# Performance work log

Hardware: AMD Instinct MI355X
Metric: run time of the kernel (lower is better)

## Reference

```python
import jax, jax.numpy as jnp
import numpy as np

B, S, HID = 2, 2048, 2048
NH, NKV, HD = 8, 2, 256
EPS = 1e-6
ROPE_THETA = 1e6


def _rms_norm(x, w):
    # Gemma3nRMSNorm: computed in fp32, x / sqrt(mean(x^2) + eps) * w
    xf = x.astype(jnp.float32)
    out = xf * jax.lax.rsqrt(jnp.mean(xf * xf, axis=-1, keepdims=True) + EPS) * w
    return out.astype(x.dtype)


def _rotate_half(x):
    x1, x2 = jnp.split(x, 2, axis=-1)
    return jnp.concatenate((-x2, x1), axis=-1)


def _apply_rope(x, cos, sin):
    # x: [B, S, H, D]; cos/sin: [B, S, D] -> unsqueeze head dim (unsqueeze_dim=2)
    c = cos[:, :, None, :]
    s = sin[:, :, None, :]
    return x * c + _rotate_half(x) * s


def setup_inputs() -> dict:
    key = jax.random.key(0)
    ks = jax.random.split(key, 6)
    hidden_states = jax.random.normal(ks[0], (B, S, HID), dtype=jnp.float32)
    # RoPE tables (theta = 1e6, Gemma3n)
    inv_freq = 1.0 / (ROPE_THETA ** (np.arange(0, HD, 2, dtype=np.float32) / HD))
    pos = np.arange(S, dtype=np.float32)
    freqs = pos[:, None] * inv_freq[None, :]            # [S, D/2]
    emb = np.concatenate([freqs, freqs], axis=-1)        # [S, D]
    cos = jnp.broadcast_to(jnp.asarray(np.cos(emb)), (B, S, HD)).astype(jnp.float32)
    sin = jnp.broadcast_to(jnp.asarray(np.sin(emb)), (B, S, HD)).astype(jnp.float32)
    # additive causal mask [B, 1, S, S]
    causal = jnp.tril(jnp.ones((S, S), dtype=bool))
    attention_mask = jnp.where(causal, 0.0, -1e9).astype(jnp.float32)
    attention_mask = jnp.broadcast_to(attention_mask[None, None], (B, 1, S, S))
    std = 0.02
    Wq = jax.random.normal(ks[1], (NH * HD, HID), dtype=jnp.float32) * std
    Wk = jax.random.normal(ks[2], (NKV * HD, HID), dtype=jnp.float32) * std
    Wv = jax.random.normal(ks[3], (NKV * HD, HID), dtype=jnp.float32) * std
    Wo = jax.random.normal(ks[4], (HID, NH * HD), dtype=jnp.float32) * std
    q_norm_w = jnp.ones((HD,), dtype=jnp.float32)
    k_norm_w = jnp.ones((HD,), dtype=jnp.float32)
    return {
        "hidden_states": hidden_states, "cos": cos, "sin": sin,
        "attention_mask": attention_mask,
        "Wq": Wq, "Wk": Wk, "Wv": Wv, "Wo": Wo,
        "q_norm_w": q_norm_w, "k_norm_w": k_norm_w,
    }


def reference(hidden_states, cos, sin, attention_mask, Wq, Wk, Wv, Wo, q_norm_w, k_norm_w):
    b, s, _ = hidden_states.shape
    # projections (no bias)
    q = (hidden_states @ Wq.T).reshape(b, s, NH, HD)
    k = (hidden_states @ Wk.T).reshape(b, s, NKV, HD)
    v = (hidden_states @ Wv.T).reshape(b, s, NKV, HD)
    # QK-norm then RoPE; v_norm has no scale (weight = 1)
    q = _apply_rope(_rms_norm(q, q_norm_w), cos, sin)
    k = _apply_rope(_rms_norm(k, k_norm_w), cos, sin)
    v = _rms_norm(v, jnp.float32(1.0))
    q = q.transpose(0, 2, 1, 3)  # [B, NH, S, D]
    k = k.transpose(0, 2, 1, 3)  # [B, NKV, S, D]
    v = v.transpose(0, 2, 1, 3)
    # repeat_kv: NKV -> NH (n_rep = NH // NKV)
    n_rep = NH // NKV
    k = jnp.repeat(k, n_rep, axis=1)
    v = jnp.repeat(v, n_rep, axis=1)
    # eager attention, scaling = 1.0 (as in Gemma3nTextAttention), no softcap
    scores = jnp.einsum("bhqd,bhkd->bhqk", q, k) + attention_mask
    probs = jax.nn.softmax(scores.astype(jnp.float32), axis=-1).astype(q.dtype)
    out = jnp.einsum("bhqk,bhkd->bqhd", probs, v).reshape(b, s, NH * HD)
    return out @ Wo.T
```

## Files before the change

kernel.cpp:

```cpp
#include <hip/hip_runtime.h>
#include <hip/hip_bf16.h>
#include <stdint.h>

#define S_LEN 2048
#define HIDN  2048
#define NH    8
#define NKV   2
#define HD    256

typedef _Float16 v8h  __attribute__((ext_vector_type(8)));
typedef float    v4f  __attribute__((ext_vector_type(4)));
typedef float    v16f __attribute__((ext_vector_type(16)));
typedef unsigned short u16;

struct alignas(8) US4 { u16 x, y, z, w; };

__device__ __forceinline__ u16 f2h(float f) {
  union { _Float16 h; u16 u; } t; t.h = (_Float16)f; return t.u;
}
__device__ __forceinline__ float h2f(u16 u) {
  union { _Float16 h; u16 u; } t; t.u = u; return (float)t.h;
}
__device__ __forceinline__ uint32_t pk2(float a, float b) {
  return (uint32_t)f2h(a) | ((uint32_t)f2h(b) << 16);
}

template <typename T>
__device__ __forceinline__ void gload16(const T* g, void* l) {
  __builtin_amdgcn_global_load_lds(
      (const __attribute__((address_space(1))) void*)g,
      (__attribute__((address_space(3))) void*)l, 16, 0, 0);
}

__device__ __forceinline__ void cvt_quad(const float* src, u16* dst) {
  float4 v = *reinterpret_cast<const float4*>(src);
  US4 o; o.x = f2h(v.x); o.y = f2h(v.y); o.z = f2h(v.z); o.w = f2h(v.w);
  *reinterpret_cast<US4*>(dst) = o;
}

__global__ void cvt_all_kernel(
    const float* __restrict__ hs, const float* __restrict__ Wq,
    const float* __restrict__ Wk, const float* __restrict__ Wv,
    const float* __restrict__ Wo,
    u16* __restrict__ hs_f, u16* __restrict__ w_f, u16* __restrict__ wo_f) {
  int j = blockIdx.x * blockDim.x + threadIdx.x;
  if (j < 2097152) { cvt_quad(hs + (size_t)j * 4, hs_f + (size_t)j * 4); return; }
  j -= 2097152;
  if (j < 1048576) { cvt_quad(Wq + (size_t)j * 4, w_f + (size_t)j * 4); return; }
  j -= 1048576;
  if (j < 262144) { cvt_quad(Wk + (size_t)j * 4, w_f + 4194304 + (size_t)j * 4); return; }
  j -= 262144;
  if (j < 262144) { cvt_quad(Wv + (size_t)j * 4, w_f + 5242880 + (size_t)j * 4); return; }
  j -= 262144;
  cvt_quad(Wo + (size_t)j * 4, wo_f + (size_t)j * 4);
}

template <int MF, int NFR, int OUT_F16>
__global__ __launch_bounds__(512, 2) void gemm256(
    const u16* __restrict__ A, const u16* __restrict__ Bm,
    void* __restrict__ C, int M, int N, int K) {
  __shared__ u16 As[2][MF * 2048];
  __shared__ u16 Bs[2][NFR * 4096];
  const int tid = threadIdx.x;
  const int w = tid >> 6, lane = tid & 63;
  const int wm = w >> 2, wn = w & 3;
  const int lr = lane & 15, ls = lane >> 4;
  const int m0 = blockIdx.x * (MF * 32);
  const int n0 = blockIdx.y * (NFR * 64);
  const int KT = K >> 6;
  constexpr int FPP = MF / 4;
  v4f acc[MF][NFR] = {};

  auto stageA = [&](int kt, int buf, int r) {
    const int idx = r * 512 + tid;
    const int row = idx >> 3, sp = idx & 7;
    const int sl = sp ^ (row & 7);
    gload16(A + (size_t)(m0 + row) * K + kt * 64 + sl * 8, (char*)As[buf] + idx * 16);
  };
  auto stageB = [&](int kt, int buf, int r) {
    const int idx = r * 512 + tid;
    const int row = idx >> 3, sp = idx & 7;
    const int sl = sp ^ (row & 7);
    gload16(Bm + (size_t)(n0 + row) * K + kt * 64 + sl * 8, (char*)Bs[buf] + idx * 16);
  };

#pragma unroll
  for (int r = 0; r < MF / 2; r++) stageA(0, 0, r);
#pragma unroll
  for (int r = 0; r < NFR; r++) stageB(0, 0, r);
  asm volatile("s_waitcnt vmcnt(0)" ::: "memory");
  __builtin_amdgcn_s_barrier();
  __builtin_amdgcn_sched_barrier(0);

  for (int kt = 0; kt < KT; kt++) {
    const int buf = kt & 1;
    v8h bfrag[2][NFR];
#pragma unroll
    for (int p = 0; p < 4; p++) {
      if (p == 0) {
#pragma unroll
        for (int kk = 0; kk < 2; kk++)
#pragma unroll
          for (int j = 0; j < NFR; j++) {
            const int row = wn * (NFR * 16) + j * 16 + lr;
            const int sp = (kk * 4 + ls) ^ (row & 7);
            bfrag[kk][j] = *reinterpret_cast<const v8h*>(&Bs[buf][row * 64 + sp * 8]);
          }
      }
      v8h a2[FPP][2];
#pragma unroll
      for (int ii = 0; ii < FPP; ii++)
#pragma unroll
        for (int kk = 0; kk < 2; kk++) {
          const int row = wm * MF * 16 + (p * FPP + ii) * 16 + lr;
          const int sp = (kk * 4 + ls) ^ (row & 7);
          a2[ii][kk] = *reinterpret_cast<const v8h*>(&As[buf][row * 64 + sp * 8]);
        }
      if (kt + 1 < KT) {
        if (p == 0) {
#pragma unroll
          for (int r = 0; r < MF / 2; r++) stageA(kt + 1, buf ^ 1, r);
        }
        if (p == 1) {
#pragma unroll
          for (int r = 0; r < NFR; r++) stageB(kt + 1, buf ^ 1, r);
        }
      }
      if (p == 3) asm volatile("s_waitcnt vmcnt(0)" ::: "memory");
      __builtin_amdgcn_s_barrier();
      asm volatile("s_waitcnt lgkmcnt(0)" ::: "memory");
      __builtin_amdgcn_sched_barrier(0);
      __builtin_amdgcn_s_setprio(1);
#pragma unroll
      for (int ii = 0; ii < FPP; ii++)
#pragma unroll
        for (int j = 0; j < NFR; j++)
#pragma unroll
          for (int kk = 0; kk < 2; kk++)
            acc[p * FPP + ii][j] = __builtin_amdgcn_mfma_f32_16x16x32_f16(
                a2[ii][kk], bfrag[kk][j], acc[p * FPP + ii][j], 0, 0, 0);
      __builtin_amdgcn_s_setprio(0);
      __builtin_amdgcn_s_barrier();
    }
  }

#pragma unroll
  for (int i = 0; i < MF; i++)
#pragma unroll
    for (int j = 0; j < NFR; j++) {
      const int col = n0 + wn * (NFR * 16) + j * 16 + lr;
#pragma unroll
      for (int jj = 0; jj < 4; jj++) {
        const int row = m0 + wm * MF * 16 + i * 16 + ls * 4 + jj;
        if (OUT_F16) ((u16*)C)[(size_t)row * N + col] = f2h(acc[i][j][jj]);
        else         ((float*)C)[(size_t)row * N + col] = acc[i][j][jj];
      }
    }
}

__global__ __launch_bounds__(256, 4) void norm_rope_kernel(
    const u16* __restrict__ qkv, const float* __restrict__ cosb, const float* __restrict__ sinb,
    const float* __restrict__ qw, const float* __restrict__ kw,
    u16* __restrict__ q_t, u16* __restrict__ k_t, u16* __restrict__ v_t) {
  const int task = blockIdx.x * 4 + (threadIdx.x >> 6);
  const int lane = threadIdx.x & 63;
  const int unit = task % 12;
  const int ms = task / 12;
  const int b = ms >> 11, s = ms & 2047;
  const int d0 = lane << 2;
  const int col0 = (unit < 8) ? unit * 256 : 2048 + (unit - 8) * 256;
  const US4 xv = *reinterpret_cast<const US4*>(qkv + (size_t)ms * 3072 + col0 + d0);
  float x[4] = { h2f(xv.x), h2f(xv.y), h2f(xv.z), h2f(xv.w) };
  float ss = x[0]*x[0] + x[1]*x[1] + x[2]*x[2] + x[3]*x[3];
#pragma unroll
  for (int m = 1; m < 64; m <<= 1) ss += __shfl_xor(ss, m, 64);
  const float r = rsqrtf(ss * (1.0f / 256.0f) + 1e-6f);
  if (unit < 10) {
    const float4 wv = *reinterpret_cast<const float4*>(((unit < 8) ? qw : kw) + d0);
    float xn[4];
    xn[0] = x[0] * r * wv.x; xn[1] = x[1] * r * wv.y;
    xn[2] = x[2] * r * wv.z; xn[3] = x[3] * r * wv.w;
    float rot[4];
#pragma unroll
    for (int j = 0; j < 4; j++) {
      const float p = __shfl(xn[j], lane ^ 32, 64);
      rot[j] = (lane < 32) ? -p : p;
    }
    const float4 c  = *reinterpret_cast<const float4*>(cosb + (size_t)ms * 256 + d0);
    const float4 sn = *reinterpret_cast<const float4*>(sinb + (size_t)ms * 256 + d0);
    US4 o;
    o.x = f2h(xn[0] * c.x + rot[0] * sn.x);
    o.y = f2h(xn[1] * c.y + rot[1] * sn.y);
    o.z = f2h(xn[2] * c.z + rot[2] * sn.z);
    o.w = f2h(xn[3] * c.w + rot[3] * sn.w);
    if (unit < 8) {
      const size_t dst = ((size_t)(b * NH + unit) * S_LEN + s) * 256 + d0;
      *reinterpret_cast<US4*>(q_t + dst) = o;
    } else {
      const size_t dst = ((size_t)(b * NKV + (unit - 8)) * S_LEN + s) * 256 + d0;
      *reinterpret_cast<US4*>(k_t + dst) = o;
    }
  } else {
    const int kvh = unit - 10;
    u16* vt = v_t + (size_t)(b * NKV + kvh) * 256 * 2048;
#pragma unroll
    for (int j = 0; j < 4; j++)
      vt[(size_t)(d0 + j) * 2048 + s] = f2h(x[j] * r);
  }
}

__device__ __forceinline__ void stage_kv(
    const u16* __restrict__ kb, const u16* __restrict__ vb, int kt,
    u16* Kbuf, u16* Vbuf, int tid) {
#pragma unroll
  for (int it = 0; it < 4; it++) {
    const int i1 = tid + it * 512;
    const int kv = i1 >> 5, sp = i1 & 31;
    const int sl = sp ^ (kv & 31);
    gload16(kb + (size_t)(kt * 64 + kv) * 256 + sl * 8, (char*)Kbuf + i1 * 16);
    const int d = i1 >> 3, sp2 = i1 & 7;
    const int sl2 = sp2 ^ ((d >> 2) & 7);
    gload16(vb + (size_t)d * 2048 + kt * 64 + sl2 * 8, (char*)Vbuf + i1 * 16);
  }
}

__global__ __launch_bounds__(512, 2) void attn_kernel(
    const u16* __restrict__ q_t, const u16* __restrict__ k_t,
    const u16* __restrict__ v_t, u16* __restrict__ oP, float2* __restrict__ ml) {
  const int qtA = blockIdx.x;
  const int qtB = 15 - qtA;
  const int bh = blockIdx.y;
  const int b = bh >> 3, h = bh & 7, hk = h >> 2;
  const int tid = threadIdx.x;
  const int w = tid >> 6, lane = tid & 63;
  const int g = w >> 1, hf = w & 1;
  const int l31 = lane & 31, hi = lane >> 5;

  __shared__ u16 Kb[2][16384];
  __shared__ u16 Vb[2][16384];

  const u16* qhead = q_t + (size_t)(b * NH + h) * S_LEN * 256;
  const u16* kb = k_t + (size_t)(b * NKV + hk) * S_LEN * 256;
  const u16* vb = v_t + (size_t)(b * NKV + hk) * 256 * S_LEN;

  const u16* qbA = qhead + (size_t)(qtA * 128 + g * 32 + l31) * 256;
  v8h qf[16];
#pragma unroll
  for (int f = 0; f < 16; f++)
    qf[f] = *reinterpret_cast<const v8h*>(qbA + f * 16 + hi * 8);

  v16f o[4] = {};
  float mr = -1e30f, lsum = 0.f;
  int qt_cur = qtA;

  const int nA = qtA + 1;

  stage_kv(kb, vb, 0, Kb[0], Vb[0], tid);

  for (int s = 0; s < 17; s++) {
    const int cb = s & 1;
    const int kt = (s < nA) ? s : (qtB + 1 + s - nA);
    if (s + 1 < 17) {
      const int s1 = s + 1;
      const int ktn = (s1 < nA) ? s1 : (qtB + 1 + s1 - nA);
      stage_kv(kb, vb, ktn, Kb[cb ^ 1], Vb[cb ^ 1], tid);
      asm volatile("s_waitcnt vmcnt(8)" ::: "memory");
    } else {
      asm volatile("s_waitcnt vmcnt(0)" ::: "memory");
    }
    __builtin_amdgcn_s_barrier();
    __builtin_amdgcn_sched_barrier(0);

    if (s == nA) {
      const size_t rowi = (((size_t)bh) * 16 + qtA) * 128 + g * 32 + l31;
      u16* ob = oP + rowi * 256;
#pragma unroll
      for (int dblk = 0; dblk < 4; dblk++)
#pragma unroll
        for (int rr = 0; rr < 4; rr++) {
          const int dbase = hf * 128 + dblk * 32 + rr * 8 + hi * 4;
          uint2 pw;
          pw.x = pk2(o[dblk][rr * 4 + 0], o[dblk][rr * 4 + 1]);
          pw.y = pk2(o[dblk][rr * 4 + 2], o[dblk][rr * 4 + 3]);
          *reinterpret_cast<uint2*>(ob + dbase) = pw;
        }
      if (hf == 0 && lane < 32)
        ml[rowi] = make_float2(mr, lsum);
      const u16* qbB = qhead + (size_t)(qtB * 128 + g * 32 + l31) * 256;
#pragma unroll
      for (int f = 0; f < 16; f++)
        qf[f] = *reinterpret_cast<const v8h*>(qbB + f * 16 + hi * 8);
#pragma unroll
      for (int dblk = 0; dblk < 4; dblk++) o[dblk] = v16f{};
      mr = -1e30f; lsum = 0.f;
      qt_cur = qtB;
    }

    v16f s0 = {}, s1 = {};
    __builtin_amdgcn_s_setprio(1);
#pragma unroll
    for (int ds = 0; ds < 16; ds++) {
      const int sp = (ds * 2 + hi) ^ l31;
      const v8h kf0 = *reinterpret_cast<const v8h*>(&Kb[cb][l31 * 256 + sp * 8]);
      const v8h kf1 = *reinterpret_cast<const v8h*>(&Kb[cb][(32 + l31) * 256 + sp * 8]);
      s0 = __builtin_amdgcn_mfma_f32_32x32x16_f16(kf0, qf[ds], s0, 0, 0, 0);
      s1 = __builtin_amdgcn_mfma_f32_32x32x16_f16(kf1, qf[ds], s1, 0, 0, 0);
    }
    __builtin_amdgcn_s_setprio(0);
    if (kt >= 2 * qt_cur) {
      const int qg = qt_cur * 128 + g * 32 + l31;
#pragma unroll
      for (int r = 0; r < 16; r++) {
        const int kvr = kt * 64 + (r & 3) + 8 * (r >> 2) + 4 * hi;
        if (kvr > qg) s0[r] = -1e30f;
        if (kvr + 32 > qg) s1[r] = -1e30f;
      }
    }
    float pm = s0[0];
#pragma unroll
    for (int r = 1; r < 16; r++) pm = fmaxf(pm, s0[r]);
#pragma unroll
    for (int r = 0; r < 16; r++) pm = fmaxf(pm, s1[r]);
    pm = fmaxf(pm, __shfl_xor(pm, 32, 64));
    if (!__all(pm - mr <= 8.0f)) {
      const float mn = fmaxf(mr, pm);
      const float sc = __expf(mr - mn);
      mr = mn;
      lsum *= sc;
#pragma unroll
      for (int dblk = 0; dblk < 4; dblk++)
#pragma unroll
        for (int r = 0; r < 16; r++) o[dblk][r] *= sc;
    }
    float rs = 0.f;
#pragma unroll
    for (int r = 0; r < 16; r++) { s0[r] = __expf(s0[r] - mr); rs += s0[r]; }
#pragma unroll
    for (int r = 0; r < 16; r++) { s1[r] = __expf(s1[r] - mr); rs += s1[r]; }
    rs += __shfl_xor(rs, 32, 64);
    lsum += rs;
    uint32_t pka[2][8], pkx[2][8];
#pragma unroll
    for (int u = 0; u < 8; u++) {
      const int r = (u & 1) * 2 + (u >> 1) * 4;
      pka[0][u] = pk2(s0[r], s0[r + 1]);
      pka[1][u] = pk2(s1[r], s1[r + 1]);
    }
#pragma unroll
    for (int n = 0; n < 2; n++)
#pragma unroll
      for (int u = 0; u < 8; u++)
        pkx[n][u] = (uint32_t)__shfl_xor((int)pka[n][u], 32, 64);
    v8h bfr[4];
#pragma unroll
    for (int sblk = 0; sblk < 4; sblk++) {
      const int n = sblk >> 1, base = (sblk & 1) * 4;
      union { uint32_t u[4]; v8h h; } t;
      if (hi == 0) {
        t.u[0] = pka[n][base];     t.u[1] = pka[n][base + 1];
        t.u[2] = pkx[n][base];     t.u[3] = pkx[n][base + 1];
      } else {
        t.u[0] = pkx[n][base + 2]; t.u[1] = pkx[n][base + 3];
        t.u[2] = pka[n][base + 2]; t.u[3] = pka[n][base + 3];
      }
      bfr[sblk] = t.h;
    }
    __builtin_amdgcn_s_setprio(1);
#pragma unroll
    for (int dblk = 0; dblk < 4; dblk++) {
      const int d = hf * 128 + dblk * 32 + l31;
#pragma unroll
      for (int sblk = 0; sblk < 4; sblk++) {
        const int sp = (sblk * 2 + hi) ^ ((d >> 2) & 7);
        const v8h vf = *reinterpret_cast<const v8h*>(&Vb[cb][d * 64 + sp * 8]);
        o[dblk] = __builtin_amdgcn_mfma_f32_32x32x16_f16(vf, bfr[sblk], o[dblk], 0, 0, 0);
      }
    }
    __builtin_amdgcn_s_setprio(0);
    __builtin_amdgcn_s_barrier();
    __builtin_amdgcn_sched_barrier(0);
  }

  const size_t rowi = (((size_t)(16 + bh)) * 16 + qtB) * 128 + g * 32 + l31;
  u16* ob = oP + rowi * 256;
#pragma unroll
  for (int dblk = 0; dblk < 4; dblk++)
#pragma unroll
    for (int rr = 0; rr < 4; rr++) {
      const int dbase = hf * 128 + dblk * 32 + rr * 8 + hi * 4;
      uint2 pw;
      pw.x = pk2(o[dblk][rr * 4 + 0], o[dblk][rr * 4 + 1]);
      pw.y = pk2(o[dblk][rr * 4 + 2], o[dblk][rr * 4 + 3]);
      *reinterpret_cast<uint2*>(ob + dbase) = pw;
    }
  if (hf == 0 && lane < 32)
    ml[rowi] = make_float2(mr, lsum);
}

__global__ __launch_bounds__(256, 8) void combine_kernel(
    const u16* __restrict__ oP, const float2* __restrict__ ml,
    u16* __restrict__ aout) {
  const int wid = threadIdx.x >> 6, lane = threadIdx.x & 63;
  const int R = blockIdx.x * 4 + wid;
  const int bh = R >> 11, rem = R & 2047, qt = rem >> 7, row = rem & 127;
  const int b = bh >> 3, h = bh & 7;
  const size_t i0 = (((size_t)bh)      * 16 + qt) * 128 + row;
  const size_t i1 = (((size_t)(16+bh)) * 16 + qt) * 128 + row;
  const float2 m0 = ml[i0], m1 = ml[i1];
  const float ms = fmaxf(m0.x, m1.x);
  const float f0 = __expf(m0.x - ms), f1 = __expf(m1.x - ms);
  const float inv = 1.0f / (m0.y * f0 + m1.y * f1);
  const US4 a = reinterpret_cast<const US4*>(oP + i0 * 256)[lane];
  const US4 c = reinterpret_cast<const US4*>(oP + i1 * 256)[lane];
  US4 o;
  o.x = f2h((h2f(a.x) * f0 + h2f(c.x) * f1) * inv);
  o.y = f2h((h2f(a.y) * f0 + h2f(c.y) * f1) * inv);
  o.z = f2h((h2f(a.z) * f0 + h2f(c.z) * f1) * inv);
  o.w = f2h((h2f(a.w) * f0 + h2f(c.w) * f1) * inv);
  u16* dst = aout + ((size_t)(b * 2048 + qt * 128 + row)) * 2048 + h * 256 + lane * 4;
  *reinterpret_cast<US4*>(dst) = o;
}

extern "C" void kernel_launch(void* const* d_in, const int* in_sizes, int n_in,
                              void* d_out, int out_size, void* d_ws, size_t ws_size,
                              hipStream_t stream) {
  const float* hs   = (const float*)d_in[0];
  const float* cosb = (const float*)d_in[1];
  const float* sinb = (const float*)d_in[2];
  const float* Wq = (const float*)d_in[4];
  const float* Wk = (const float*)d_in[5];
  const float* Wv = (const float*)d_in[6];
  const float* Wo = (const float*)d_in[7];
  const float* qw = (const float*)d_in[8];
  const float* kw = (const float*)d_in[9];
  float* out = (float*)d_out;

  char* ws = (char*)d_ws;
  u16* hs_f = (u16*)(ws + 0);
  u16* w_f  = (u16*)(ws + 16777216);
  u16* wo_f = (u16*)(ws + 29360128);
  u16* qkvh = (u16*)(ws + 37748736);
  u16* q_t  = (u16*)(ws + 88080384);
  u16* k_t  = (u16*)(ws + 104857600);
  u16* v_t  = (u16*)(ws + 109051904);
  u16* oP   = (u16*)(ws + 37748736);
  float2* mlp = (float2*)(ws + 71303168);
  u16* aout = (u16*)(ws + 0);

  cvt_all_kernel<<<18432, 256, 0, stream>>>(hs, Wq, Wk, Wv, Wo, hs_f, w_f, wo_f);

  gemm256<8, 3, 1><<<dim3(16, 16), 512, 0, stream>>>(hs_f, w_f, qkvh, 4096, 3072, 2048);
  norm_rope_kernel<<<12288, 256, 0, stream>>>(qkvh, cosb, sinb, qw, kw, q_t, k_t, v_t);
  attn_kernel<<<dim3(16, 16), 512, 0, stream>>>(q_t, k_t, v_t, oP, mlp);
  combine_kernel<<<8192, 256, 0, stream>>>(oP, mlp, aout);
  gemm256<4, 4, 0><<<dim3(32, 8), 512, 0, stream>>>(aout, wo_f, out, 4096, 2048, 2048);
}
```

Baseline: 230.2 us.

## Split QK^T across wave pairs and exchange softmax stats and P via LDS

Before this change, each wave in a pair computed the full 64-key score tile, duplicating the QK^T MFMAs and the exp work across both waves. Now each wave computes only its 32-key half and exchanges row max, row sum and the packed probability fragments with its partner through shared memory. This halves the score MFMAs and the softmax arithmetic per wave. The cost is two extra block-wide barriers per KV tile and some additional LDS traffic, which could stall the pipelining between waves.

```diff
diff --git a/kernel.cpp b/kernel.cpp
--- a/kernel.cpp
+++ b/kernel.cpp
@@ -238,6 +238,9 @@
 
   __shared__ u16 Kb[2][16384];
   __shared__ u16 Vb[2][16384];
+  __shared__ v8h Pex[4][2][2][64];
+  __shared__ float Mex[4][2][32];
+  __shared__ float Lex[4][2][32];
 
   const u16* qhead = q_t + (size_t)(b * NH + h) * S_LEN * 256;
   const u16* kb = k_t + (size_t)(b * NKV + hk) * S_LEN * 256;
@@ -296,32 +299,33 @@
       qt_cur = qtB;
     }
 
-    v16f s0 = {}, s1 = {};
+    v16f s0 = {};
     __builtin_amdgcn_s_setprio(1);
 #pragma unroll
     for (int ds = 0; ds < 16; ds++) {
       const int sp = (ds * 2 + hi) ^ l31;
-      const v8h kf0 = *reinterpret_cast<const v8h*>(&Kb[cb][l31 * 256 + sp * 8]);
-      const v8h kf1 = *reinterpret_cast<const v8h*>(&Kb[cb][(32 + l31) * 256 + sp * 8]);
+      const v8h kf0 = *reinterpret_cast<const v8h*>(&Kb[cb][(hf * 32 + l31) * 256 + sp * 8]);
       s0 = __builtin_amdgcn_mfma_f32_32x32x16_f16(kf0, qf[ds], s0, 0, 0, 0);
-      s1 = __builtin_amdgcn_mfma_f32_32x32x16_f16(kf1, qf[ds], s1, 0, 0, 0);
     }
     __builtin_amdgcn_s_setprio(0);
     if (kt >= 2 * qt_cur) {
       const int qg = qt_cur * 128 + g * 32 + l31;
 #pragma unroll
       for (int r = 0; r < 16; r++) {
-        const int kvr = kt * 64 + (r & 3) + 8 * (r >> 2) + 4 * hi;
+        const int kvr = kt * 64 + hf * 32 + (r & 3) + 8 * (r >> 2) + 4 * hi;
         if (kvr > qg) s0[r] = -1e30f;
-        if (kvr + 32 > qg) s1[r] = -1e30f;
-      }
-    }
-    float pm = s0[0];
-#pragma unroll
-    for (int r = 1; r < 16; r++) pm = fmaxf(pm, s0[r]);
-#pragma unroll
-    for (int r = 0; r < 16; r++) pm = fmaxf(pm, s1[r]);
+      }
+    }
+    float m4[4];
+#pragma unroll
+    for (int q4 = 0; q4 < 4; q4++)
+      m4[q4] = fmaxf(fmaxf(s0[q4 * 4], s0[q4 * 4 + 1]),
+                     fmaxf(s0[q4 * 4 + 2], s0[q4 * 4 + 3]));
+    float pm = fmaxf(fmaxf(m4[0], m4[1]), fmaxf(m4[2], m4[3]));
     pm = fmaxf(pm, __shfl_xor(pm, 32, 64));
+    if (lane < 32) Mex[g][hf][l31] = pm;
+    __builtin_amdgcn_s_barrier();
+    pm = fmaxf(pm, Mex[g][hf ^ 1][l31]);
     if (!__all(pm - mr <= 8.0f)) {
       const float mn = fmaxf(mr, pm);
       const float sc = __expf(mr - mn);
@@ -332,39 +336,47 @@
 #pragma unroll
         for (int r = 0; r < 16; r++) o[dblk][r] *= sc;
     }
-    float rs = 0.f;
-#pragma unroll
-    for (int r = 0; r < 16; r++) { s0[r] = __expf(s0[r] - mr); rs += s0[r]; }
-#pragma unroll
-    for (int r = 0; r < 16; r++) { s1[r] = __expf(s1[r] - mr); rs += s1[r]; }
+#pragma unroll
+    for (int r = 0; r < 16; r++) s0[r] = __expf(s0[r] - mr);
+    float t4[4];
+#pragma unroll
+    for (int q4 = 0; q4 < 4; q4++)
+      t4[q4] = (s0[q4 * 4] + s0[q4 * 4 + 1]) + (s0[q4 * 4 + 2] + s0[q4 * 4 + 3]);
+    float rs = (t4[0] + t4[1]) + (t4[2] + t4[3]);
     rs += __shfl_xor(rs, 32, 64);
-    lsum += rs;
-    uint32_t pka[2][8], pkx[2][8];
+    uint32_t pka[8], pkx[8];
 #pragma unroll
     for (int u = 0; u < 8; u++) {
       const int r = (u & 1) * 2 + (u >> 1) * 4;
-      pka[0][u] = pk2(s0[r], s0[r + 1]);
-      pka[1][u] = pk2(s1[r], s1[r + 1]);
-    }
-#pragma unroll
-    for (int n = 0; n < 2; n++)
-#pragma unroll
-      for (int u = 0; u < 8; u++)
-        pkx[n][u] = (uint32_t)__shfl_xor((int)pka[n][u], 32, 64);
-    v8h bfr[4];
-#pragma unroll
-    for (int sblk = 0; sblk < 4; sblk++) {
-      const int n = sblk >> 1, base = (sblk & 1) * 4;
+      pka[u] = pk2(s0[r], s0[r + 1]);
+    }
+#pragma unroll
+    for (int u = 0; u < 8; u++)
+      pkx[u] = (uint32_t)__shfl_xor((int)pka[u], 32, 64);
+    v8h own2[2];
+#pragma unroll
+    for (int s2 = 0; s2 < 2; s2++) {
+      const int base = s2 * 4;
       union { uint32_t u[4]; v8h h; } t;
       if (hi == 0) {
-        t.u[0] = pka[n][base];     t.u[1] = pka[n][base + 1];
-        t.u[2] = pkx[n][base];     t.u[3] = pkx[n][base + 1];
+        t.u[0] = pka[base];     t.u[1] = pka[base + 1];
+        t.u[2] = pkx[base];     t.u[3] = pkx[base + 1];
       } else {
-        t.u[0] = pkx[n][base + 2]; t.u[1] = pkx[n][base + 3];
-        t.u[2] = pka[n][base + 2]; t.u[3] = pka[n][base + 3];
-      }
-      bfr[sblk] = t.h;
-    }
+        t.u[0] = pkx[base + 2]; t.u[1] = pkx[base + 3];
+        t.u[2] = pka[base + 2]; t.u[3] = pka[base + 3];
+      }
+      own2[s2] = t.h;
+    }
+    if (lane < 32) Lex[g][hf][l31] = rs;
+    Pex[g][hf][0][lane] = own2[0];
+    Pex[g][hf][1][lane] = own2[1];
+    __builtin_amdgcn_s_barrier();
+    lsum += rs + Lex[g][hf ^ 1][l31];
+    v8h bfr[4];
+    bfr[hf * 2 + 0] = own2[0];
+    bfr[hf * 2 + 1] = own2[1];
+    bfr[(hf ^ 1) * 2 + 0] = Pex[g][hf ^ 1][0][lane];
+    bfr[(hf ^ 1) * 2 + 1] = Pex[g][hf ^ 1][1][lane];
     __builtin_amdgcn_s_setprio(1);
 #pragma unroll
     for (int dblk = 0; dblk < 4; dblk++) {
```

New measurement: 353.9 us. 1.54x slower.
